# Performance work log

Hardware: AMD Instinct MI355X
Metric: run time of the kernel (lower is better)

The kernel has to match this reference:

```python
import jax, jax.numpy as jnp
import numpy as np

ACOUSTIC_BOOKS = [1, 2, 3, 4, 5, 6, 7, 8, 9, 10, 11, 12, 13, 14, 15, 16, 17, 17, 17, 17, 17]


def setup_inputs() -> dict:
    key = jax.random.key(0)
    ks = jax.random.split(key, 6)
    B, C, T, D, K, NB = 4, 512, 4096, 256, 2048, 18
    return {
        "x": jax.random.normal(ks[0], (B, C, T), dtype=jnp.float32),
        "Win_s": jax.random.normal(ks[1], (D, C), dtype=jnp.float32) * 0.05,
        "Win_a": jax.random.normal(ks[2], (D, C), dtype=jnp.float32) * 0.05,
        "Wout_s": jax.random.normal(ks[3], (C, D), dtype=jnp.float32) * 0.05,
        "Wout_a": jax.random.normal(ks[4], (C, D), dtype=jnp.float32) * 0.05,
        "E": jax.random.normal(ks[5], (NB, K, D), dtype=jnp.float32),
    }


def _nearest(z, e):
    # z: [B, D, T], e: [K, D] -> codes [B, T] via argmin of squared euclidean dist
    zt = z.transpose(0, 2, 1)  # [B, T, D]
    d2 = (jnp.sum(zt * zt, axis=-1, keepdims=True)
          - 2.0 * jnp.einsum('btd,kd->btk', zt, e)
          + jnp.sum(e * e, axis=-1))  # [B, T, K]
    return jnp.argmin(d2, axis=-1)  # [B, T]


def reference(x, Win_s, Win_a, Wout_s, Wout_a, E):
    # ---- encode ----
    xs = jnp.einsum('dc,bct->bdt', Win_s, x)  # in_proj_s (1x1 conv, no bias)
    codes = [_nearest(xs, E[0])]
    xa = jnp.einsum('dc,bct->bdt', Win_a, x)  # in_proj_a
    for cb in ACOUSTIC_BOOKS:
        idx = _nearest(xa, E[cb])
        xa = xa - E[cb][idx].transpose(0, 2, 1)  # residual subtract (decode gather)
        codes.append(idx)
    codes = jnp.stack(codes, axis=1)  # [B, 22, T]

    # ---- decode ----
    semantic = E[0][codes[:, 0]].transpose(0, 2, 1)  # [B, D, T]
    acoustic = jnp.zeros_like(semantic)
    for i, cb in enumerate(ACOUSTIC_BOOKS):
        acoustic = acoustic + E[cb][codes[:, i + 1]].transpose(0, 2, 1)
    out = (jnp.einsum('cd,bdt->bct', Wout_s, semantic)
           + jnp.einsum('cd,bdt->bct', Wout_a, acoustic))  # [B, 512, T]
    return out, codes
```

## Files before the change

### kernel.cpp

```cpp
#include <hip/hip_runtime.h>
#include <float.h>

#define TT 4096
#define BB 4
#define CC 512
#define DD 256
#define KK 2048
#define MM (BB*TT)
#define NBOOKS 22
#define EPS_PAIR 0.5f
#define EPS_FULL 0.5f
#define ZSTR 352
#define RPB 32

typedef _Float16 half8_t __attribute__((ext_vector_type(8)));
typedef float f32x4 __attribute__((ext_vector_type(4)));

__device__ __forceinline__ uint32_t packsc(float s, int code) {
  uint32_t b = __float_as_uint(s);
  uint32_t key = b ^ ((uint32_t)((int32_t)b >> 31) | 0x80000000u);
  return (key & 0xFFFFF800u) | (uint32_t)code;
}
__device__ __forceinline__ float unpacksc(uint32_t p) {
  uint32_t key = p & 0xFFFFF800u;
  uint32_t b = (key & 0x80000000u) ? (key ^ 0x80000000u) : ~key;
  return __uint_as_float(b);
}
__device__ __forceinline__ void ins3(uint32_t& v1, uint32_t& v2, uint32_t& v3,
                                     uint32_t p) {
  uint32_t t1 = max(v1, p); v1 = min(v1, p);
  uint32_t t2 = max(v2, t1); v2 = min(v2, t1);
  v3 = min(v3, t2);
}

__global__ __launch_bounds__(256) void proj_kernel(const float* __restrict__ x,
    const float* __restrict__ Ws, const float* __restrict__ Wa,
    float* __restrict__ xs, float* __restrict__ xa)
{
  __shared__ float xt[16*64];
  __shared__ float wsl[16*68];
  __shared__ float wal[16*68];
  const int tid = threadIdx.x;
  const int t0 = blockIdx.x*64, d0 = blockIdx.y*64, b = blockIdx.z;
  const int u = tid & 63, cq = tid >> 6;
  const int tx = tid & 15, ty = tid >> 4;
  const float* xb = x + (size_t)b*CC*TT;
  float accS[4][4] = {{0}}, accA[4][4] = {{0}};
  for (int c0 = 0; c0 < CC; c0 += 16) {
    __syncthreads();
    #pragma unroll
    for (int i = 0; i < 4; ++i) {
      int cc = cq*4 + i;
      xt[cc*64 + u] = xb[(size_t)(c0+cc)*TT + t0 + u];
    }
    {
      float4 wv = *(const float4*)&Ws[(size_t)(d0+u)*CC + c0 + cq*4];
      wsl[(cq*4+0)*68 + u] = wv.x; wsl[(cq*4+1)*68 + u] = wv.y;
      wsl[(cq*4+2)*68 + u] = wv.z; wsl[(cq*4+3)*68 + u] = wv.w;
      wv = *(const float4*)&Wa[(size_t)(d0+u)*CC + c0 + cq*4];
      wal[(cq*4+0)*68 + u] = wv.x; wal[(cq*4+1)*68 + u] = wv.y;
      wal[(cq*4+2)*68 + u] = wv.z; wal[(cq*4+3)*68 + u] = wv.w;
    }
    __syncthreads();
    #pragma unroll
    for (int cc = 0; cc < 16; ++cc) {
      float4 tq = *(const float4*)&xt[cc*64 + ty*4];
      float4 sq = *(const float4*)&wsl[cc*68 + tx*4];
      float4 aq = *(const float4*)&wal[cc*68 + tx*4];
      float tf[4] = {tq.x,tq.y,tq.z,tq.w};
      float sf[4] = {sq.x,sq.y,sq.z,sq.w};
      float af[4] = {aq.x,aq.y,aq.z,aq.w};
      #pragma unroll
      for (int i = 0; i < 4; ++i)
        #pragma unroll
        for (int j = 0; j < 4; ++j) {
          accS[i][j] = fmaf(tf[i], sf[j], accS[i][j]);
          accA[i][j] = fmaf(tf[i], af[j], accA[i][j]);
        }
    }
  }
  #pragma unroll
  for (int i = 0; i < 4; ++i) {
    size_t r = (size_t)b*TT + t0 + ty*4 + i;
    float4 o;
    o.x = accS[i][0]; o.y = accS[i][1]; o.z = accS[i][2]; o.w = accS[i][3];
    *(float4*)&xs[r*DD + d0 + tx*4] = o;
    o.x = accA[i][0]; o.y = accA[i][1]; o.z = accA[i][2]; o.w = accA[i][3];
    *(float4*)&xa[r*DD + d0 + tx*4] = o;
  }
}

__global__ __launch_bounds__(256) void e2_kernel(const float* __restrict__ E,
    float* __restrict__ e2)
{
  int gid = blockIdx.x*256 + threadIdx.x;
  int wid = gid >> 6, lane = gid & 63;
  if (wid < 18*KK) {
    float4 v = *(const float4*)&E[(size_t)wid*DD + lane*4];
    float s = v.x*v.x + v.y*v.y + v.z*v.z + v.w*v.w;
    #pragma unroll
    for (int m = 1; m <= 32; m <<= 1) s += __shfl_xor(s, m);
    if (lane == 0) e2[wid] = s;
  }
}

__global__ __launch_bounds__(256) void cvt_e16_kernel(const float* __restrict__ E,
    _Float16* __restrict__ E16)
{
  size_t i = ((size_t)blockIdx.x*256 + threadIdx.x)*8;
  float4 u = *(const float4*)&E[i];
  float4 v = *(const float4*)&E[i+4];
  half8_t h;
  h[0]=(_Float16)u.x; h[1]=(_Float16)u.y; h[2]=(_Float16)u.z; h[3]=(_Float16)u.w;
  h[4]=(_Float16)v.x; h[5]=(_Float16)v.y; h[6]=(_Float16)v.z; h[7]=(_Float16)v.w;
  *(half8_t*)&E16[i] = h;
}

__global__ __launch_bounds__(256) __attribute__((amdgpu_waves_per_eu(3,3)))
void fused_encode_kernel(
    const float* __restrict__ xs_g, const float* __restrict__ xa_g,
    const float* __restrict__ E, const _Float16* __restrict__ E16,
    const float* __restrict__ e2, int* __restrict__ codes0,
    float* __restrict__ codes_f, float* __restrict__ aco_g)
{
  const int tid = threadIdx.x;
  const int lane = tid & 63, wave = tid >> 6;
  const int ln15 = lane & 15, lq = lane >> 4;
  const int row0 = blockIdx.x * RPB;

  __shared__ float Z[RPB][ZSTR];
  __shared__ uint32_t L1[4][RPB], L2[4][RPB], L3[4][RPB];
  __shared__ int   codes_s[RPB];
  __shared__ int   flist[RPB], plist[RPB];
  __shared__ int   nfull, npair;
  __shared__ double Rv[4];
  __shared__ int    Ri[4];

  const int ldr = tid & 31, cg = tid >> 5;
  const int sr = tid >> 3, sg = tid & 7;

  for (int ib = 0; ib < NBOOKS; ++ib) {
    const int book = (ib <= 17) ? ib : 17;
    const float*     Eb   = E   + (size_t)book*KK*DD;
    const _Float16*  E16b = E16 + (size_t)book*KK*DD;
    const float*     e2b  = e2  + (size_t)book*KK;

    if (ib <= 1) {
      const float* src = (ib == 0) ? xs_g : xa_g;
      const float* sp = src + (size_t)(row0 + ldr)*DD + cg*32;
      #pragma unroll
      for (int j = 0; j < 8; ++j)
        *(float4*)&Z[ldr][cg*32 + j*4] = *(const float4*)(sp + j*4);
    }
    if (tid == 0) { nfull = 0; npair = 0; }
    __syncthreads();

    half8_t A[2][8];
    #pragma unroll
    for (int mt = 0; mt < 2; ++mt) {
      #pragma unroll
      for (int ks = 0; ks < 8; ++ks) {
        const float* zp = &Z[mt*16 + ln15][lq*8 + ks*32];
        float4 u = *(const float4*)zp;
        float4 v = *(const float4*)(zp + 4);
        half8_t a;
        a[0]=(_Float16)u.x; a[1]=(_Float16)u.y; a[2]=(_Float16)u.z; a[3]=(_Float16)u.w;
        a[4]=(_Float16)v.x; a[5]=(_Float16)v.y; a[6]=(_Float16)v.z; a[7]=(_Float16)v.w;
        A[mt][ks] = a;
      }
    }

    uint32_t p1[2][4], p2[2][4], p3[2][4];
    #pragma unroll
    for (int mt = 0; mt < 2; ++mt)
      #pragma unroll
      for (int j = 0; j < 4; ++j) {
        p1[mt][j] = 0xFFFFFFFFu; p2[mt][j] = 0xFFFFFFFFu; p3[mt][j] = 0xFFFFFFFFu;
      }

    const _Float16* ebase = E16b + (size_t)(wave*512 + ln15)*DD + lq*8;

    for (int nt = 0; nt < 32; ++nt) {
      const _Float16* bp = ebase + (size_t)nt*16*DD;
      half8_t B[8];
      #pragma unroll
      for (int ks = 0; ks < 8; ++ks) B[ks] = *(const half8_t*)(bp + ks*32);
      int code = wave*512 + nt*16 + ln15;
      float e2v = e2b[code];
      f32x4 acc[2];
      #pragma unroll
      for (int mt = 0; mt < 2; ++mt) acc[mt] = (f32x4){0.f,0.f,0.f,0.f};
      #pragma unroll
      for (int ks = 0; ks < 8; ++ks) {
        #pragma unroll
        for (int mt = 0; mt < 2; ++mt)
          acc[mt] = __builtin_amdgcn_mfma_f32_16x16x32_f16(A[mt][ks], B[ks], acc[mt], 0, 0, 0);
      }
      #pragma unroll
      for (int mt = 0; mt < 2; ++mt)
        #pragma unroll
        for (int j = 0; j < 4; ++j) {
          float u = fmaf(-2.f, acc[mt][j], e2v);
          ins3(p1[mt][j], p2[mt][j], p3[mt][j], packsc(u, code));
        }
    }

    #pragma unroll
    for (int mt = 0; mt < 2; ++mt)
      #pragma unroll
      for (int j = 0; j < 4; ++j) {
        uint32_t v1 = p1[mt][j], v2 = p2[mt][j], v3 = p3[mt][j];
        #pragma unroll
        for (int m = 1; m <= 8; m <<= 1) {
          uint32_t w1 = (uint32_t)__shfl_xor((int)v1, m);
          uint32_t w2 = (uint32_t)__shfl_xor((int)v2, m);
          uint32_t w3 = (uint32_t)__shfl_xor((int)v3, m);
          ins3(v1, v2, v3, w1);
          ins3(v1, v2, v3, w2);
          ins3(v1, v2, v3, w3);
        }
        if (ln15 == 0) {
          int rl = mt*16 + lq*4 + j;
          L1[wave][rl] = v1; L2[wave][rl] = v2; L3[wave][rl] = v3;
        }
      }
    __syncthreads();
    if (tid < RPB) {
      uint32_t v1 = L1[0][tid], v2 = L2[0][tid], v3 = L3[0][tid];
      #pragma unroll
      for (int w = 1; w < 4; ++w) {
        ins3(v1, v2, v3, L1[w][tid]);
        ins3(v1, v2, v3, L2[w][tid]);
        ins3(v1, v2, v3, L3[w][tid]);
      }
      int a1 = (int)(v1 & 2047u), a2 = (int)(v2 & 2047u);
      float f1 = unpacksc(v1), f2 = unpacksc(v2), f3 = unpacksc(v3);
      codes_s[tid] = a1;
      int rg = row0 + tid;
      codes_f[((size_t)(rg >> 12)*NBOOKS + ib)*TT + (rg & (TT-1))] = (float)a1;
      if (ib == 0) codes0[rg] = a1;
      if (f3 - f1 < EPS_FULL) {
        flist[atomicAdd(&nfull, 1)] = tid;
      } else if (f2 - f1 < EPS_PAIR) {
        plist[atomicAdd(&npair, 1)] = tid | (a1 << 6) | (a2 << 17);
      }
    }
    __syncthreads();

    int nfl = nfull;
    for (int f = 0; f < nfl; ++f) {
      int row = flist[f];
      double bestv = DBL_MAX; int besti = 0x7fffffff;
      #pragma unroll
      for (int q = 0; q < 8; ++q) {
        int k = q*256 + tid;
        const float* er = Eb + (size_t)k*DD;
        double s = 0.0;
        for (int d = 0; d < DD; d += 4) {
          float4 e = *(const float4*)(er + d);
          double d0 = (double)Z[row][d+0] - (double)e.x; s += d0*d0;
          double d1 = (double)Z[row][d+1] - (double)e.y; s += d1*d1;
          double d2 = (double)Z[row][d+2] - (double)e.z; s += d2*d2;
          double d3 = (double)Z[row][d+3] - (double)e.w; s += d3*d3;
        }
        if (s < bestv || (s == bestv && k < besti)) { bestv = s; besti = k; }
      }
      #pragma unroll
      for (int m = 1; m <= 32; m <<= 1) {
        double ov = __shfl_xor(bestv, m);
        int    oi = __shfl_xor(besti, m);
        if (ov < bestv || (ov == bestv && oi < besti)) { bestv = ov; besti = oi; }
      }
      if (lane == 0) { Rv[wave] = bestv; Ri[wave] = besti; }
      __syncthreads();
      if (tid == 0) {
        double bvv = Rv[0]; int bii = Ri[0];
        #pragma unroll
        for (int w = 1; w < 4; ++w)
          if (Rv[w] < bvv || (Rv[w] == bvv && Ri[w] < bii)) { bvv = Rv[w]; bii = Ri[w]; }
        codes_s[row] = bii;
        int rg = row0 + row;
        codes_f[((size_t)(rg >> 12)*NBOOKS + ib)*TT + (rg & (TT-1))] = (float)bii;
        if (ib == 0) codes0[rg] = bii;
      }
      __syncthreads();
    }

    {
      int npr = npair;
      for (int f = wave; f < npr; f += 4) {
        int pk = plist[f];
        int row = pk & 63;
        int c1 = (pk >> 6) & 2047, c2 = (pk >> 17) & 2047;
        int cc = (lane < 32) ? c1 : c2;
        const float* er = Eb + (size_t)cc*DD + (lane & 31)*8;
        const float* zr = &Z[row][(lane & 31)*8];
        double s = 0.0;
        #pragma unroll
        for (int d = 0; d < 8; ++d) {
          double df = (double)zr[d] - (double)er[d];
          s += df*df;
        }
        #pragma unroll
        for (int m = 1; m <= 16; m <<= 1) s += __shfl_xor(s, m);
        double so = __shfl_xor(s, 32);
        double d1 = (lane < 32) ? s : so;
        double d2 = (lane < 32) ? so : s;
        int win = (d2 < d1 || (d2 == d1 && c2 < c1)) ? c2 : c1;
        if (lane == 0) {
          codes_s[row] = win;
          int rg = row0 + row;
          codes_f[((size_t)(rg >> 12)*NBOOKS + ib)*TT + (rg & (TT-1))] = (float)win;
          if (ib == 0) codes0[rg] = win;
        }
      }
    }
    __syncthreads();

    if (ib >= 1) {
      int code = codes_s[sr];
      const float* er = Eb + (size_t)code*DD;
      #pragma unroll
      for (int j = 0; j < 8; ++j) {
        int c = sg*4 + j*32;
        float4 e = *(const float4*)(er + c);
        float4 z = *(const float4*)&Z[sr][c];
        z.x -= e.x; z.y -= e.y; z.z -= e.z; z.w -= e.w;
        *(float4*)&Z[sr][c] = z;
      }
    }
    __syncthreads();
  }

  {
    const float* xp = xa_g + (size_t)(row0 + ldr)*DD + cg*32;
    float*       ap = aco_g + (size_t)(row0 + ldr)*DD + cg*32;
    #pragma unroll
    for (int j = 0; j < 8; ++j) {
      float4 x0 = *(const float4*)(xp + j*4);
      float4 zf = *(const float4*)&Z[ldr][cg*32 + j*4];
      float4 o;
      o.x = x0.x - zf.x; o.y = x0.y - zf.y; o.z = x0.z - zf.z; o.w = x0.w - zf.w;
      *(float4*)(ap + j*4) = o;
    }
  }
}

__global__ __launch_bounds__(256) void final_kernel(
    const float* __restrict__ Wos, const float* __restrict__ Woa,
    const float* __restrict__ E0, const int* __restrict__ codes0,
    const float* __restrict__ aco, float* __restrict__ out)
{
  __shared__ float wsl[16*68], wal[16*68], sml[16*68], acl[16*68];
  const int tid = threadIdx.x;
  const int t0 = blockIdx.x*64, c0 = blockIdx.y*64, b = blockIdx.z;
  const int u = tid & 63, dq = tid >> 6;
  const int tx = tid & 15, ty = tid >> 4;
  int code = codes0[b*TT + t0 + u];
  const float* smr = E0 + (size_t)code*DD;
  const float* acr = aco + (size_t)(b*TT + t0 + u)*DD;
  const float* wsr = Wos + (size_t)(c0+u)*DD;
  const float* war = Woa + (size_t)(c0+u)*DD;
  float accS[4][4] = {{0}}, accA[4][4] = {{0}};
  for (int dc0 = 0; dc0 < DD; dc0 += 16) {
    __syncthreads();
    float4 v;
    v = *(const float4*)(wsr + dc0 + dq*4);
    wsl[(dq*4+0)*68+u]=v.x; wsl[(dq*4+1)*68+u]=v.y; wsl[(dq*4+2)*68+u]=v.z; wsl[(dq*4+3)*68+u]=v.w;
    v = *(const float4*)(war + dc0 + dq*4);
    wal[(dq*4+0)*68+u]=v.x; wal[(dq*4+1)*68+u]=v.y; wal[(dq*4+2)*68+u]=v.z; wal[(dq*4+3)*68+u]=v.w;
    v = *(const float4*)(smr + dc0 + dq*4);
    sml[(dq*4+0)*68+u]=v.x; sml[(dq*4+1)*68+u]=v.y; sml[(dq*4+2)*68+u]=v.z; sml[(dq*4+3)*68+u]=v.w;
    v = *(const float4*)(acr + dc0 + dq*4);
    acl[(dq*4+0)*68+u]=v.x; acl[(dq*4+1)*68+u]=v.y; acl[(dq*4+2)*68+u]=v.z; acl[(dq*4+3)*68+u]=v.w;
    __syncthreads();
    #pragma unroll
    for (int d = 0; d < 16; ++d) {
      float4 cs = *(const float4*)&wsl[d*68 + tx*4];
      float4 ca = *(const float4*)&wal[d*68 + tx*4];
      float4 ts = *(const float4*)&sml[d*68 + ty*4];
      float4 ta = *(const float4*)&acl[d*68 + ty*4];
      float csf[4]={cs.x,cs.y,cs.z,cs.w}, caf[4]={ca.x,ca.y,ca.z,ca.w};
      float tsf[4]={ts.x,ts.y,ts.z,ts.w}, taf[4]={ta.x,ta.y,ta.z,ta.w};
      #pragma unroll
      for (int i = 0; i < 4; ++i)
        #pragma unroll
        for (int j = 0; j < 4; ++j) {
          accS[i][j] = fmaf(csf[i], tsf[j], accS[i][j]);
          accA[i][j] = fmaf(caf[i], taf[j], accA[i][j]);
        }
    }
  }
  size_t ob = (size_t)b*CC*TT;
  #pragma unroll
  for (int i = 0; i < 4; ++i) {
    float4 r;
    r.x = accS[i][0] + accA[i][0];
    r.y = accS[i][1] + accA[i][1];
    r.z = accS[i][2] + accA[i][2];
    r.w = accS[i][3] + accA[i][3];
    *(float4*)&out[ob + (size_t)(c0 + tx*4 + i)*TT + t0 + ty*4] = r;
  }
}

extern "C" void kernel_launch(void* const* d_in, const int* in_sizes, int n_in,
                              void* d_out, int out_size, void* d_ws, size_t ws_size,
                              hipStream_t stream) {
  const float* x    = (const float*)d_in[0];
  const float* Wins = (const float*)d_in[1];
  const float* Wina = (const float*)d_in[2];
  const float* Wos  = (const float*)d_in[3];
  const float* Woa  = (const float*)d_in[4];
  const float* E    = (const float*)d_in[5];
  float* out = (float*)d_out;
  float* codes_f = out + (size_t)BB*CC*TT;

  _Float16* E16 = (_Float16*)d_out;

  float* xs  = (float*)d_ws;
  float* xa  = xs + (size_t)MM*DD;
  float* aco = xa + (size_t)MM*DD;
  float* e2  = aco + (size_t)MM*DD;
  int* codes_i = (int*)(e2 + 18*KK);

  proj_kernel<<<dim3(TT/64, DD/64, BB), 256, 0, stream>>>(x, Wins, Wina, xs, xa);
  e2_kernel<<<(18*KK*64)/256, 256, 0, stream>>>(E, e2);
  cvt_e16_kernel<<<(18*KK*DD)/8/256, 256, 0, stream>>>(E, E16);

  fused_encode_kernel<<<MM/RPB, 256, 0, stream>>>(xs, xa, E, E16, e2,
                                                  codes_i, codes_f, aco);

  final_kernel<<<dim3(TT/64, CC/64, BB), 256, 0, stream>>>(Wos, Woa, E, codes_i, aco, out);
}
```

Baseline: 1.953 ms.

## Double-buffer codebook tile loads, stage e2 in LDS, shrink Z stride

```diff
diff --git a/kernel.cpp b/kernel.cpp
--- a/kernel.cpp
+++ b/kernel.cpp
@@ -10,7 +10,7 @@
 #define NBOOKS 22
 #define EPS_PAIR 0.5f
 #define EPS_FULL 0.5f
-#define ZSTR 352
+#define ZSTR 260
 #define RPB 32
 
 typedef _Float16 half8_t __attribute__((ext_vector_type(8)));
@@ -116,7 +116,27 @@
   *(half8_t*)&E16[i] = h;
 }
 
-__global__ __launch_bounds__(256) __attribute__((amdgpu_waves_per_eu(3,3)))
+__device__ __forceinline__ void tile_compute(
+    const half8_t A[2][8], const half8_t B[8], float e2v, int code,
+    uint32_t p1[2][4], uint32_t p2[2][4], uint32_t p3[2][4])
+{
+  f32x4 a0 = (f32x4){0.f,0.f,0.f,0.f};
+  f32x4 a1 = (f32x4){0.f,0.f,0.f,0.f};
+  #pragma unroll
+  for (int ks = 0; ks < 8; ++ks) {
+    a0 = __builtin_amdgcn_mfma_f32_16x16x32_f16(A[0][ks], B[ks], a0, 0, 0, 0);
+    a1 = __builtin_amdgcn_mfma_f32_16x16x32_f16(A[1][ks], B[ks], a1, 0, 0, 0);
+  }
+  #pragma unroll
+  for (int j = 0; j < 4; ++j) {
+    float u0 = fmaf(-2.f, a0[j], e2v);
+    ins3(p1[0][j], p2[0][j], p3[0][j], packsc(u0, code));
+    float u1 = fmaf(-2.f, a1[j], e2v);
+    ins3(p1[1][j], p2[1][j], p3[1][j], packsc(u1, code));
+  }
+}
+
+__global__ __launch_bounds__(256) __attribute__((amdgpu_waves_per_eu(1)))
 void fused_encode_kernel(
     const float* __restrict__ xs_g, const float* __restrict__ xa_g,
     const float* __restrict__ E, const _Float16* __restrict__ E16,
@@ -129,6 +149,7 @@
   const int row0 = blockIdx.x * RPB;
 
   __shared__ float Z[RPB][ZSTR];
+  __shared__ float e2s[KK];
   __shared__ uint32_t L1[4][RPB], L2[4][RPB], L3[4][RPB];
   __shared__ int   codes_s[RPB];
   __shared__ int   flist[RPB], plist[RPB];
@@ -151,6 +172,10 @@
       #pragma unroll
       for (int j = 0; j < 8; ++j)
         *(float4*)&Z[ldr][cg*32 + j*4] = *(const float4*)(sp + j*4);
+    }
+    {
+      *(float4*)&e2s[tid*8]     = *(const float4*)&e2b[tid*8];
+      *(float4*)&e2s[tid*8 + 4] = *(const float4*)&e2b[tid*8 + 4];
     }
     if (tid == 0) { nfull = 0; npair = 0; }
     __syncthreads();
@@ -180,29 +205,26 @@
 
     const _Float16* ebase = E16b + (size_t)(wave*512 + ln15)*DD + lq*8;
 
-    for (int nt = 0; nt < 32; ++nt) {
-      const _Float16* bp = ebase + (size_t)nt*16*DD;
-      half8_t B[8];
-      #pragma unroll
-      for (int ks = 0; ks < 8; ++ks) B[ks] = *(const half8_t*)(bp + ks*32);
-      int code = wave*512 + nt*16 + ln15;
-      float e2v = e2b[code];
-      f32x4 acc[2];
-      #pragma unroll
-      for (int mt = 0; mt < 2; ++mt) acc[mt] = (f32x4){0.f,0.f,0.f,0.f};
-      #pragma unroll
-      for (int ks = 0; ks < 8; ++ks) {
-        #pragma unroll
-        for (int mt = 0; mt < 2; ++mt)
-          acc[mt] = __builtin_amdgcn_mfma_f32_16x16x32_f16(A[mt][ks], B[ks], acc[mt], 0, 0, 0);
-      }
-      #pragma unroll
-      for (int mt = 0; mt < 2; ++mt)
-        #pragma unroll
-        for (int j = 0; j < 4; ++j) {
-          float u = fmaf(-2.f, acc[mt][j], e2v);
-          ins3(p1[mt][j], p2[mt][j], p3[mt][j], packsc(u, code));
-        }
+    half8_t B0[8], B1[8];
+    #pragma unroll
+    for (int ks = 0; ks < 8; ++ks) B0[ks] = *(const half8_t*)(ebase + ks*32);
+
+    for (int nt = 0; nt < 32; nt += 2) {
+      const _Float16* bp1 = ebase + (size_t)(nt+1)*16*DD;
+      #pragma unroll
+      for (int ks = 0; ks < 8; ++ks) B1[ks] = *(const half8_t*)(bp1 + ks*32);
+
+      int code0 = wave*512 + nt*16 + ln15;
+      tile_compute(A, B0, e2s[code0], code0, p1, p2, p3);
+
+      if (nt + 2 < 32) {
+        const _Float16* bp2 = ebase + (size_t)(nt+2)*16*DD;
+        #pragma unroll
+        for (int ks = 0; ks < 8; ++ks) B0[ks] = *(const half8_t*)(bp2 + ks*32);
+      }
+
+      int code1 = wave*512 + (nt+1)*16 + ln15;
+      tile_compute(A, B1, e2s[code1], code1, p1, p2, p3);
     }
 
     #pragma unroll
```

Result: slower. 2.001 ms (+2.5%).
